# Kernel optimization log

Hardware: AMD Instinct MI355X
Metric: run time of the kernel (lower is better)

The kernel has to match this reference:

```python
import jax, jax.numpy as jnp
import numpy as np

SCALE = 0.0078125  # dequant scale from init_kwargs


def setup_inputs() -> dict:
    key = jax.random.key(0)
    k1, k2, k3 = jax.random.split(key, 3)
    B, S, D_IN, D_OUT = 4, 2048, 2048, 8192
    x = jax.random.normal(k1, (B, S, D_IN), dtype=jnp.float32)
    weight = jax.random.normal(k2, (D_OUT, D_IN), dtype=jnp.float32)  # torch Linear layout
    bias = jax.random.normal(k3, (D_OUT,), dtype=jnp.float32)
    return {"x": x, "weight": weight, "bias": bias}


def reference(x, weight, bias):
    # MATMUL.apply(x, weight.t(), bias, scale): scaled matmul + fused bias
    # out[b,s,o] = scale * sum_i x[b,s,i] * weight[o,i] + bias[o]
    out = jnp.einsum('bsi,oi->bso', x, weight) * jnp.asarray(SCALE, x.dtype)
    return out + bias
```

## Files before the change

kernel.cpp:

```cpp
#include <hip/hip_runtime.h>
#include <hip/hip_bf16.h>
#include <stdint.h>

typedef __bf16 bf16x8 __attribute__((ext_vector_type(8)));
typedef float  f32x4  __attribute__((ext_vector_type(4)));

static constexpr float kScale = 0.0078125f;

static __device__ __forceinline__ uint32_t bf16_rne(float f) {
  uint32_t u = __builtin_bit_cast(uint32_t, f);
  u += 0x7FFFu + ((u >> 16) & 1u);
  return u >> 16;
}
static __device__ __forceinline__ uint32_t pack2(float lo, float hi) {
  return bf16_rne(lo) | (bf16_rne(hi) << 16);
}

__global__ __launch_bounds__(256) void cvt_f32_to_bf16(
    const float* __restrict__ src, uint4* __restrict__ dst) {
  const int i = blockIdx.x * 256 + threadIdx.x;
  const float4* sv = reinterpret_cast<const float4*>(src);
  float4 a = sv[2 * i];
  float4 b = sv[2 * i + 1];
  uint4 o;
  o.x = pack2(a.x, a.y);
  o.y = pack2(a.z, a.w);
  o.z = pack2(b.x, b.y);
  o.w = pack2(b.z, b.w);
  dst[i] = o;
}

static __device__ __forceinline__ void gload_lds16(const void* g, void* l) {
  __builtin_amdgcn_global_load_lds(
      (const __attribute__((address_space(1))) void*)g,
      (__attribute__((address_space(3))) void*)l, 16, 0, 0);
}

#define BARRIER() __builtin_amdgcn_s_barrier()
#define LGKM0()                                        \
  do {                                                 \
    asm volatile("s_waitcnt lgkmcnt(0)" ::: "memory"); \
    __builtin_amdgcn_sched_barrier(0);                 \
  } while (0)
#define VM6()                                          \
  do {                                                 \
    asm volatile("s_waitcnt vmcnt(6)" ::: "memory");   \
    __builtin_amdgcn_sched_barrier(0);                 \
  } while (0)

template <int MH, int NH>
__device__ __forceinline__ void quad(f32x4 (&acc)[8][4],
                                     const bf16x8 (&aF)[4][2],
                                     const bf16x8 (&bF)[2][2]) {
#pragma unroll
  for (int mi = 0; mi < 4; ++mi)
#pragma unroll
    for (int ni = 0; ni < 2; ++ni)
#pragma unroll
      for (int kk = 0; kk < 2; ++kk)
        acc[MH * 4 + mi][NH * 2 + ni] = __builtin_amdgcn_mfma_f32_16x16x32_bf16(
            aF[mi][kk], bF[ni][kk], acc[MH * 4 + mi][NH * 2 + ni], 0, 0, 0);
}

__global__ __launch_bounds__(512, 2) void gemm256_8phase(
    const uint16_t* __restrict__ A, const uint16_t* __restrict__ B,
    const float* __restrict__ bias, float* __restrict__ C,
    int Mi, int Ni, int Ki) {
  __shared__ __align__(16) uint16_t As[2][256 * 64];
  __shared__ __align__(16) uint16_t Bs[2][256 * 64];

  const int tid = threadIdx.x;
  const int l   = tid & 63;
  const int wv  = tid >> 6;
  const int wr  = wv >> 2;
  const int wc  = wv & 3;
  const int fr  = l & 15;
  const int fh  = l >> 4;
  const int l8  = l >> 3;
  const int l7  = l & 7;

  const int nbm = Mi >> 8, nbn = Ni >> 8;
  const int nwg = nbm * nbn;
  const int q = nwg >> 3, r = nwg & 7;
  const int xcd = (int)blockIdx.x & 7, orig = (int)blockIdx.x >> 3;
  const int swz = (xcd < r ? xcd * (q + 1) : r * (q + 1) + (xcd - r) * q) + orig;
  const int bm = swz / nbn;
  const int bn = swz % nbn;

  const int xcol = (l7 ^ l8) << 3;
  const uint16_t* gA0 = A + (size_t)((bm << 8) + (wv << 3) + l8) * Ki + xcol;
  const int bw0 = ((wv & 3) << 3) + ((wv >> 2) << 6);
  const uint16_t* gB0 = B + (size_t)((bn << 8) + bw0 + l8) * Ki + xcol;

#define STAGE_A(bufi, chunk, t)                              \
  gload_lds16(gA0 + (size_t)(chunk) * Ki + (t) * 64,         \
              &As[bufi][(size_t)((chunk) + (wv << 3)) << 6])
#define STAGE_B(bufi, roff, t)                               \
  gload_lds16(gB0 + (size_t)(roff) * Ki + (t) * 64,          \
              &Bs[bufi][(size_t)(bw0 + (roff)) << 6])

  const int ac0 = fh ^ (fr & 7);
  const bf16x8* Av = reinterpret_cast<const bf16x8*>(&As[0][0]);
  const bf16x8* Bv = reinterpret_cast<const bf16x8*>(&Bs[0][0]);
  constexpr int TILE_V = (256 * 64) / 8;

#define LDA_(bufi, mh, mi, kk)                                              \
  Av[(bufi) * TILE_V + (((wr << 7) + ((mh) << 6) + ((mi) << 4) + fr) << 3) + \
     (ac0 ^ ((kk) << 2))]
#define LDB_(bufi, nh, ni, kk)                                              \
  Bv[(bufi) * TILE_V + (((wc << 6) + ((nh) << 5) + ((ni) << 4) + fr) << 3) + \
     (ac0 ^ ((kk) << 2))]

  f32x4 acc[8][4] = {};
  bf16x8 aF[4][2], b0[2][2], b1[2][2];

  const int NT = Ki >> 6;
  const int NI = NT >> 1;

  STAGE_A(0, 0, 0);
  STAGE_B(0, 0, 0);
  STAGE_A(0, 128, 0);
  STAGE_B(0, 128, 0);
  STAGE_B(0, 32, 0);
  STAGE_B(0, 160, 0);
  STAGE_A(0, 64, 0);
  STAGE_A(0, 192, 0);
  STAGE_A(1, 0, 1);
  STAGE_B(1, 0, 1);
  asm volatile("s_waitcnt vmcnt(6)" ::: "memory");
  __builtin_amdgcn_sched_barrier(0);
  BARRIER();

#pragma unroll 1
  for (int i = 0; i < NI; ++i) {
    const int t1 = 2 * i + 1, t2 = 2 * i + 2, t3 = 2 * i + 3;
    const bool g2 = (t2 < NT), g3 = (t3 < NT);

#pragma unroll
    for (int mi = 0; mi < 4; ++mi) {
      aF[mi][0] = LDA_(0, 0, mi, 0);
      aF[mi][1] = LDA_(0, 0, mi, 1);
    }
#pragma unroll
    for (int ni = 0; ni < 2; ++ni) {
      b0[ni][0] = LDB_(0, 0, ni, 0);
      b0[ni][1] = LDB_(0, 0, ni, 1);
    }
    STAGE_A(1, 128, t1);
    STAGE_B(1, 128, t1);
    VM6();
    BARRIER();
    LGKM0();
    __builtin_amdgcn_s_setprio(1);
    quad<0, 0>(acc, aF, b0);
    __builtin_amdgcn_s_setprio(0);
    BARRIER();

#pragma unroll
    for (int ni = 0; ni < 2; ++ni) {
      b1[ni][0] = LDB_(0, 1, ni, 0);
      b1[ni][1] = LDB_(0, 1, ni, 1);
    }
    STAGE_B(1, 32, t1);
    STAGE_B(1, 160, t1);
    VM6();
    BARRIER();
    LGKM0();
    __builtin_amdgcn_s_setprio(1);
    quad<0, 1>(acc, aF, b1);
    __builtin_amdgcn_s_setprio(0);
    BARRIER();

#pragma unroll
    for (int mi = 0; mi < 4; ++mi) {
      aF[mi][0] = LDA_(0, 1, mi, 0);
      aF[mi][1] = LDA_(0, 1, mi, 1);
    }
    STAGE_A(1, 64, t1);
    STAGE_A(1, 192, t1);
    VM6();
    BARRIER();
    LGKM0();
    __builtin_amdgcn_s_setprio(1);
    quad<1, 0>(acc, aF, b0);
    __builtin_amdgcn_s_setprio(0);
    BARRIER();

    if (g2) {
      STAGE_A(0, 0, t2);
      STAGE_B(0, 0, t2);
    }
    VM6();
    BARRIER();
    LGKM0();
    __builtin_amdgcn_s_setprio(1);
    quad<1, 1>(acc, aF, b1);
    __builtin_amdgcn_s_setprio(0);
    BARRIER();

#pragma unroll
    for (int mi = 0; mi < 4; ++mi) {
      aF[mi][0] = LDA_(1, 0, mi, 0);
      aF[mi][1] = LDA_(1, 0, mi, 1);
    }
#pragma unroll
    for (int ni = 0; ni < 2; ++ni) {
      b0[ni][0] = LDB_(1, 0, ni, 0);
      b0[ni][1] = LDB_(1, 0, ni, 1);
    }
    if (g2) {
      STAGE_A(0, 128, t2);
      STAGE_B(0, 128, t2);
    }
    VM6();
    BARRIER();
    LGKM0();
    __builtin_amdgcn_s_setprio(1);
    quad<0, 0>(acc, aF, b0);
    __builtin_amdgcn_s_setprio(0);
    BARRIER();

#pragma unroll
    for (int ni = 0; ni < 2; ++ni) {
      b1[ni][0] = LDB_(1, 1, ni, 0);
      b1[ni][1] = LDB_(1, 1, ni, 1);
    }
    if (g2) {
      STAGE_B(0, 32, t2);
      STAGE_B(0, 160, t2);
    }
    VM6();
    BARRIER();
    LGKM0();
    __builtin_amdgcn_s_setprio(1);
    quad<0, 1>(acc, aF, b1);
    __builtin_amdgcn_s_setprio(0);
    BARRIER();

#pragma unroll
    for (int mi = 0; mi < 4; ++mi) {
      aF[mi][0] = LDA_(1, 1, mi, 0);
      aF[mi][1] = LDA_(1, 1, mi, 1);
    }
    if (g2) {
      STAGE_A(0, 64, t2);
      STAGE_A(0, 192, t2);
    }
    VM6();
    BARRIER();
    LGKM0();
    __builtin_amdgcn_s_setprio(1);
    quad<1, 0>(acc, aF, b0);
    __builtin_amdgcn_s_setprio(0);
    BARRIER();

    if (g3) {
      STAGE_A(1, 0, t3);
      STAGE_B(1, 0, t3);
    }
    VM6();
    BARRIER();
    LGKM0();
    __builtin_amdgcn_s_setprio(1);
    quad<1, 1>(acc, aF, b1);
    __builtin_amdgcn_s_setprio(0);
    BARRIER();
  }

  const int rowB = (bm << 8) + (wr << 7);
  const int colB = (bn << 8) + (wc << 6);
#pragma unroll
  for (int n = 0; n < 4; ++n) {
    const int col = colB + n * 16 + fr;
    const float bv = bias[col];
#pragma unroll
    for (int m = 0; m < 8; ++m) {
      const int row = rowB + m * 16 + fh * 4;
#pragma unroll
      for (int j = 0; j < 4; ++j)
        C[(size_t)(row + j) * Ni + col] = acc[m][n][j] * kScale + bv;
    }
  }
}

__global__ __launch_bounds__(256) void gemm_bf16_bias(
    const uint16_t* __restrict__ A, const uint16_t* __restrict__ B,
    const float* __restrict__ bias, float* __restrict__ C,
    int Mi, int Ni, int Ki) {
  __shared__ __align__(16) uint16_t As[128 * 32];
  __shared__ __align__(16) uint16_t Bs[128 * 32];

  const int tid  = threadIdx.x;
  const int lane = tid & 63;
  const int wv   = tid >> 6;
  const int wr   = wv >> 1;
  const int wc   = wv & 1;
  const int fr   = lane & 15;
  const int fh   = lane >> 4;

  const int nTilesN = Ni >> 7;
  const int nwg = gridDim.x;
  const int q = nwg >> 3, r = nwg & 7;
  const int xcd = (int)blockIdx.x & 7, orig = (int)blockIdx.x >> 3;
  const int swz = (xcd < r ? xcd * (q + 1) : r * (q + 1) + (xcd - r) * q) + orig;
  const int bm = swz / nTilesN;
  const int bn = swz % nTilesN;

  const int sRow = tid >> 2;
  const int sCol = (tid & 3) << 3;

  const uint16_t* gA0 = A + (size_t)(bm * 128 + sRow) * Ki + sCol;
  const uint16_t* gA1 = gA0 + (size_t)64 * Ki;
  const uint16_t* gB0 = B + (size_t)(bn * 128 + sRow) * Ki + sCol;
  const uint16_t* gB1 = gB0 + (size_t)64 * Ki;
  uint16_t* lA0 = &As[tid * 8];
  uint16_t* lA1 = &As[(256 + tid) * 8];
  uint16_t* lB0 = &Bs[tid * 8];
  uint16_t* lB1 = &Bs[(256 + tid) * 8];

  const bf16x8* Av = reinterpret_cast<const bf16x8*>(As);
  const bf16x8* Bv = reinterpret_cast<const bf16x8*>(Bs);

  f32x4 acc[4][4] = {};

  for (int k0 = 0; k0 < Ki; k0 += 32) {
    gload_lds16(gA0 + k0, lA0);
    gload_lds16(gA1 + k0, lA1);
    gload_lds16(gB0 + k0, lB0);
    gload_lds16(gB1 + k0, lB1);
    __syncthreads();

    bf16x8 af[4], bfr[4];
#pragma unroll
    for (int m = 0; m < 4; ++m) af[m] = Av[(wr * 64 + m * 16 + fr) * 4 + fh];
#pragma unroll
    for (int n = 0; n < 4; ++n) bfr[n] = Bv[(wc * 64 + n * 16 + fr) * 4 + fh];

#pragma unroll
    for (int m = 0; m < 4; ++m)
#pragma unroll
      for (int n = 0; n < 4; ++n)
        acc[m][n] = __builtin_amdgcn_mfma_f32_16x16x32_bf16(af[m], bfr[n],
                                                            acc[m][n], 0, 0, 0);
    __syncthreads();
  }

  const int rowBase = bm * 128 + wr * 64;
  const int colBase = bn * 128 + wc * 64;
#pragma unroll
  for (int n = 0; n < 4; ++n) {
    const int col = colBase + n * 16 + fr;
    const float bv = bias[col];
#pragma unroll
    for (int m = 0; m < 4; ++m) {
      const int row = rowBase + m * 16 + fh * 4;
#pragma unroll
      for (int j = 0; j < 4; ++j)
        C[(size_t)(row + j) * Ni + col] = acc[m][n][j] * kScale + bv;
    }
  }
}

__global__ void naive_gemm(const float* __restrict__ x, const float* __restrict__ w,
                           const float* __restrict__ bias, float* __restrict__ out,
                           int Mi, int Ni, int Ki) {
  long idx = (long)blockIdx.x * blockDim.x + threadIdx.x;
  if (idx >= (long)Mi * Ni) return;
  int m = (int)(idx / Ni), n = (int)(idx % Ni);
  float s = 0.f;
  for (int k = 0; k < Ki; ++k) s += x[(long)m * Ki + k] * w[(long)n * Ki + k];
  out[idx] = s * kScale + bias[n];
}

extern "C" void kernel_launch(void* const* d_in, const int* in_sizes, int n_in,
                              void* d_out, int out_size, void* d_ws, size_t ws_size,
                              hipStream_t stream) {
  const float* x    = (const float*)d_in[0];
  const float* w    = (const float*)d_in[1];
  const float* bias = (const float*)d_in[2];
  float* out = (float*)d_out;

  const int Ni = in_sizes[2];
  const int Ki = in_sizes[1] / Ni;
  const int Mi = in_sizes[0] / Ki;

  const size_t nx = (size_t)Mi * Ki;
  const size_t nw = (size_t)Ni * Ki;

  if (ws_size >= (nx + nw) * sizeof(uint16_t) && (Ki % 32) == 0 &&
      (Mi % 128) == 0 && (Ni % 128) == 0) {
    uint16_t* xb = (uint16_t*)d_ws;
    uint16_t* wb = xb + nx;
    cvt_f32_to_bf16<<<(int)(nx / 2048), 256, 0, stream>>>(x, (uint4*)xb);
    cvt_f32_to_bf16<<<(int)(nw / 2048), 256, 0, stream>>>(w, (uint4*)wb);

    if ((Mi % 256) == 0 && (Ni % 256) == 0 && (Ki % 128) == 0) {
      dim3 grid((Mi / 256) * (Ni / 256));
      gemm256_8phase<<<grid, 512, 0, stream>>>(xb, wb, bias, out, Mi, Ni, Ki);
    } else {
      dim3 grid((Mi / 128) * (Ni / 128));
      gemm_bf16_bias<<<grid, 256, 0, stream>>>(xb, wb, bias, out, Mi, Ni, Ki);
    }
  } else {
    long total = (long)Mi * Ni;
    naive_gemm<<<(int)((total + 255) / 256), 256, 0, stream>>>(x, w, bias, out,
                                                               Mi, Ni, Ki);
  }
}
```

Baseline: 372.5 us.

## Restructure 8-phase GEMM pipeline with interleaved warp-to-tile mapping and peeled tail

Changes each wave's sub-tile mapping so a wave covers rows and columns split across the two halves of the 256x256 tile. The global-to-LDS staging is reordered to match, loading A and B in contiguous 64-row chunks at an earlier point in the schedule. Most phases drop the vmcnt wait and use a partial lgkmcnt wait, and the final iteration is peeled so the main loop needs no guards. The aim is to let more memory traffic overlap with MFMA work and to cut wait stalls. The cost is tighter correctness margins around buffer reuse ordering.

```diff
diff --git a/kernel.cpp b/kernel.cpp
--- a/kernel.cpp
+++ b/kernel.cpp
@@ -42,16 +42,20 @@
     asm volatile("s_waitcnt lgkmcnt(0)" ::: "memory"); \
     __builtin_amdgcn_sched_barrier(0);                 \
   } while (0)
-#define VM6()                                          \
-  do {                                                 \
-    asm volatile("s_waitcnt vmcnt(6)" ::: "memory");   \
-    __builtin_amdgcn_sched_barrier(0);                 \
+#define LGKM8() asm volatile("s_waitcnt lgkmcnt(8)" ::: "memory")
+#define VMW(n)                                               \
+  do {                                                       \
+    asm volatile("s_waitcnt vmcnt(" #n ")" ::: "memory");    \
+    __builtin_amdgcn_sched_barrier(0);                       \
   } while (0)
+
+constexpr int TILE_V = (256 * 64) / 8;
 
 template <int MH, int NH>
 __device__ __forceinline__ void quad(f32x4 (&acc)[8][4],
                                      const bf16x8 (&aF)[4][2],
                                      const bf16x8 (&bF)[2][2]) {
+  __builtin_amdgcn_s_setprio(1);
 #pragma unroll
   for (int mi = 0; mi < 4; ++mi)
 #pragma unroll
@@ -60,6 +64,28 @@
       for (int kk = 0; kk < 2; ++kk)
         acc[MH * 4 + mi][NH * 2 + ni] = __builtin_amdgcn_mfma_f32_16x16x32_bf16(
             aF[mi][kk], bF[ni][kk], acc[MH * 4 + mi][NH * 2 + ni], 0, 0, 0);
+  __builtin_amdgcn_s_setprio(0);
+}
+
+template <int BUF, int MH>
+__device__ __forceinline__ void loadA(bf16x8 (&aF)[4][2], const bf16x8* Av,
+                                      int wr, int fr, int ac0) {
+#pragma unroll
+  for (int mi = 0; mi < 4; ++mi) {
+    const int row = (MH << 7) + (wr << 6) + (mi << 4) + fr;
+    aF[mi][0] = Av[BUF * TILE_V + row * 8 + ac0];
+    aF[mi][1] = Av[BUF * TILE_V + row * 8 + (ac0 ^ 4)];
+  }
+}
+template <int BUF, int NH>
+__device__ __forceinline__ void loadB(bf16x8 (&bF)[2][2], const bf16x8* Bv,
+                                      int wc, int fr, int ac0) {
+#pragma unroll
+  for (int ni = 0; ni < 2; ++ni) {
+    const int row = (NH << 7) + (wc << 5) + (ni << 4) + fr;
+    bF[ni][0] = Bv[BUF * TILE_V + row * 8 + ac0];
+    bF[ni][1] = Bv[BUF * TILE_V + row * 8 + (ac0 ^ 4)];
+  }
 }
 
 __global__ __launch_bounds__(512, 2) void gemm256_8phase(
@@ -89,27 +115,18 @@
 
   const int xcol = (l7 ^ l8) << 3;
   const uint16_t* gA0 = A + (size_t)((bm << 8) + (wv << 3) + l8) * Ki + xcol;
-  const int bw0 = ((wv & 3) << 3) + ((wv >> 2) << 6);
-  const uint16_t* gB0 = B + (size_t)((bn << 8) + bw0 + l8) * Ki + xcol;
-
-#define STAGE_A(bufi, chunk, t)                              \
-  gload_lds16(gA0 + (size_t)(chunk) * Ki + (t) * 64,         \
-              &As[bufi][(size_t)((chunk) + (wv << 3)) << 6])
-#define STAGE_B(bufi, roff, t)                               \
-  gload_lds16(gB0 + (size_t)(roff) * Ki + (t) * 64,          \
-              &Bs[bufi][(size_t)(bw0 + (roff)) << 6])
+  const uint16_t* gB0 = B + (size_t)((bn << 8) + (wv << 3) + l8) * Ki + xcol;
+
+#define STAGE_A(bufi, chunk, t)                        \
+  gload_lds16(gA0 + (size_t)(chunk) * Ki + (t) * 64,   \
+              &As[bufi][((chunk) + (wv << 3)) << 6])
+#define STAGE_B(bufi, chunk, t)                        \
+  gload_lds16(gB0 + (size_t)(chunk) * Ki + (t) * 64,   \
+              &Bs[bufi][((chunk) + (wv << 3)) << 6])
 
   const int ac0 = fh ^ (fr & 7);
   const bf16x8* Av = reinterpret_cast<const bf16x8*>(&As[0][0]);
   const bf16x8* Bv = reinterpret_cast<const bf16x8*>(&Bs[0][0]);
-  constexpr int TILE_V = (256 * 64) / 8;
-
-#define LDA_(bufi, mh, mi, kk)                                              \
-  Av[(bufi) * TILE_V + (((wr << 7) + ((mh) << 6) + ((mi) << 4) + fr) << 3) + \
-     (ac0 ^ ((kk) << 2))]
-#define LDB_(bufi, nh, ni, kk)                                              \
-  Bv[(bufi) * TILE_V + (((wc << 6) + ((nh) << 5) + ((ni) << 4) + fr) << 3) + \
-     (ac0 ^ ((kk) << 2))]
 
   f32x4 acc[8][4] = {};
   bf16x8 aF[4][2], b0[2][2], b1[2][2];
@@ -117,165 +134,119 @@
   const int NT = Ki >> 6;
   const int NI = NT >> 1;
 
-  STAGE_A(0, 0, 0);
-  STAGE_B(0, 0, 0);
-  STAGE_A(0, 128, 0);
-  STAGE_B(0, 128, 0);
-  STAGE_B(0, 32, 0);
-  STAGE_B(0, 160, 0);
-  STAGE_A(0, 64, 0);
-  STAGE_A(0, 192, 0);
-  STAGE_A(1, 0, 1);
-  STAGE_B(1, 0, 1);
-  asm volatile("s_waitcnt vmcnt(6)" ::: "memory");
-  __builtin_amdgcn_sched_barrier(0);
+  STAGE_A(0, 0, 0);   STAGE_A(0, 64, 0);
+  STAGE_B(0, 0, 0);   STAGE_B(0, 64, 0);
+  STAGE_B(0, 128, 0); STAGE_B(0, 192, 0);
+  STAGE_A(0, 128, 0); STAGE_A(0, 192, 0);
+  STAGE_A(1, 0, 1);   STAGE_A(1, 64, 1);
+  STAGE_B(1, 0, 1);   STAGE_B(1, 64, 1);
+  STAGE_B(1, 128, 1); STAGE_B(1, 192, 1);
+  VMW(6);
   BARRIER();
 
 #pragma unroll 1
-  for (int i = 0; i < NI; ++i) {
+  for (int i = 0; i < NI - 1; ++i) {
     const int t1 = 2 * i + 1, t2 = 2 * i + 2, t3 = 2 * i + 3;
-    const bool g2 = (t2 < NT), g3 = (t3 < NT);
-
-#pragma unroll
-    for (int mi = 0; mi < 4; ++mi) {
-      aF[mi][0] = LDA_(0, 0, mi, 0);
-      aF[mi][1] = LDA_(0, 0, mi, 1);
-    }
-#pragma unroll
-    for (int ni = 0; ni < 2; ++ni) {
-      b0[ni][0] = LDB_(0, 0, ni, 0);
-      b0[ni][1] = LDB_(0, 0, ni, 1);
-    }
-    STAGE_A(1, 128, t1);
-    STAGE_B(1, 128, t1);
-    VM6();
-    BARRIER();
-    LGKM0();
-    __builtin_amdgcn_s_setprio(1);
+
+    loadA<0, 0>(aF, Av, wr, fr, ac0);
+    loadB<0, 0>(b0, Bv, wc, fr, ac0);
+    STAGE_A(1, 128, t1); STAGE_A(1, 192, t1);
+    LGKM8();
+    BARRIER(); LGKM0();
     quad<0, 0>(acc, aF, b0);
-    __builtin_amdgcn_s_setprio(0);
-    BARRIER();
-
-#pragma unroll
-    for (int ni = 0; ni < 2; ++ni) {
-      b1[ni][0] = LDB_(0, 1, ni, 0);
-      b1[ni][1] = LDB_(0, 1, ni, 1);
-    }
-    STAGE_B(1, 32, t1);
-    STAGE_B(1, 160, t1);
-    VM6();
-    BARRIER();
-    LGKM0();
-    __builtin_amdgcn_s_setprio(1);
+    BARRIER();
+
+    loadB<0, 1>(b1, Bv, wc, fr, ac0);
+    STAGE_A(0, 0, t2); STAGE_A(0, 64, t2);
+    BARRIER(); LGKM0();
     quad<0, 1>(acc, aF, b1);
-    __builtin_amdgcn_s_setprio(0);
-    BARRIER();
-
-#pragma unroll
-    for (int mi = 0; mi < 4; ++mi) {
-      aF[mi][0] = LDA_(0, 1, mi, 0);
-      aF[mi][1] = LDA_(0, 1, mi, 1);
-    }
-    STAGE_A(1, 64, t1);
-    STAGE_A(1, 192, t1);
-    VM6();
-    BARRIER();
-    LGKM0();
-    __builtin_amdgcn_s_setprio(1);
+    BARRIER();
+
+    loadA<0, 1>(aF, Av, wr, fr, ac0);
+    STAGE_B(0, 0, t2); STAGE_B(0, 64, t2);
+    BARRIER(); LGKM0();
     quad<1, 0>(acc, aF, b0);
-    __builtin_amdgcn_s_setprio(0);
-    BARRIER();
-
-    if (g2) {
-      STAGE_A(0, 0, t2);
-      STAGE_B(0, 0, t2);
-    }
-    VM6();
-    BARRIER();
-    LGKM0();
-    __builtin_amdgcn_s_setprio(1);
+    BARRIER();
+
+    STAGE_B(0, 128, t2); STAGE_B(0, 192, t2);
+    VMW(6);
+    BARRIER();
     quad<1, 1>(acc, aF, b1);
-    __builtin_amdgcn_s_setprio(0);
-    BARRIER();
-
-#pragma unroll
-    for (int mi = 0; mi < 4; ++mi) {
-      aF[mi][0] = LDA_(1, 0, mi, 0);
-      aF[mi][1] = LDA_(1, 0, mi, 1);
-    }
-#pragma unroll
-    for (int ni = 0; ni < 2; ++ni) {
-      b0[ni][0] = LDB_(1, 0, ni, 0);
-      b0[ni][1] = LDB_(1, 0, ni, 1);
-    }
-    if (g2) {
-      STAGE_A(0, 128, t2);
-      STAGE_B(0, 128, t2);
-    }
-    VM6();
-    BARRIER();
-    LGKM0();
-    __builtin_amdgcn_s_setprio(1);
+    BARRIER();
+
+    loadA<1, 0>(aF, Av, wr, fr, ac0);
+    loadB<1, 0>(b0, Bv, wc, fr, ac0);
+    STAGE_A(0, 128, t2); STAGE_A(0, 192, t2);
+    LGKM8();
+    BARRIER(); LGKM0();
     quad<0, 0>(acc, aF, b0);
-    __builtin_amdgcn_s_setprio(0);
-    BARRIER();
-
-#pragma unroll
-    for (int ni = 0; ni < 2; ++ni) {
-      b1[ni][0] = LDB_(1, 1, ni, 0);
-      b1[ni][1] = LDB_(1, 1, ni, 1);
-    }
-    if (g2) {
-      STAGE_B(0, 32, t2);
-      STAGE_B(0, 160, t2);
-    }
-    VM6();
-    BARRIER();
-    LGKM0();
-    __builtin_amdgcn_s_setprio(1);
+    BARRIER();
+
+    loadB<1, 1>(b1, Bv, wc, fr, ac0);
+    STAGE_A(1, 0, t3); STAGE_A(1, 64, t3);
+    BARRIER(); LGKM0();
     quad<0, 1>(acc, aF, b1);
-    __builtin_amdgcn_s_setprio(0);
-    BARRIER();
-
-#pragma unroll
-    for (int mi = 0; mi < 4; ++mi) {
-      aF[mi][0] = LDA_(1, 1, mi, 0);
-      aF[mi][1] = LDA_(1, 1, mi, 1);
-    }
-    if (g2) {
-      STAGE_A(0, 64, t2);
-      STAGE_A(0, 192, t2);
-    }
-    VM6();
-    BARRIER();
-    LGKM0();
-    __builtin_amdgcn_s_setprio(1);
+    BARRIER();
+
+    loadA<1, 1>(aF, Av, wr, fr, ac0);
+    STAGE_B(1, 0, t3); STAGE_B(1, 64, t3);
+    BARRIER(); LGKM0();
     quad<1, 0>(acc, aF, b0);
-    __builtin_amdgcn_s_setprio(0);
-    BARRIER();
-
-    if (g3) {
-      STAGE_A(1, 0, t3);
-      STAGE_B(1, 0, t3);
-    }
-    VM6();
-    BARRIER();
-    LGKM0();
-    __builtin_amdgcn_s_setprio(1);
+    BARRIER();
+
+    STAGE_B(1, 128, t3); STAGE_B(1, 192, t3);
+    VMW(6);
+    BARRIER();
     quad<1, 1>(acc, aF, b1);
-    __builtin_amdgcn_s_setprio(0);
-    BARRIER();
-  }
-
-  const int rowB = (bm << 8) + (wr << 7);
-  const int colB = (bn << 8) + (wc << 6);
+    BARRIER();
+  }
+
+  {
+    const int t1 = NT - 1;
+    loadA<0, 0>(aF, Av, wr, fr, ac0);
+    loadB<0, 0>(b0, Bv, wc, fr, ac0);
+    STAGE_A(1, 128, t1); STAGE_A(1, 192, t1);
+    LGKM8();
+    BARRIER(); LGKM0();
+    quad<0, 0>(acc, aF, b0);
+    BARRIER();
+    loadB<0, 1>(b1, Bv, wc, fr, ac0);
+    BARRIER(); LGKM0();
+    quad<0, 1>(acc, aF, b1);
+    BARRIER();
+    loadA<0, 1>(aF, Av, wr, fr, ac0);
+    BARRIER(); LGKM0();
+    quad<1, 0>(acc, aF, b0);
+    BARRIER();
+    VMW(0);
+    BARRIER();
+    quad<1, 1>(acc, aF, b1);
+    BARRIER();
+    loadA<1, 0>(aF, Av, wr, fr, ac0);
+    loadB<1, 0>(b0, Bv, wc, fr, ac0);
+    BARRIER(); LGKM0();
+    quad<0, 0>(acc, aF, b0);
+    BARRIER();
+    loadB<1, 1>(b1, Bv, wc, fr, ac0);
+    BARRIER(); LGKM0();
+    quad<0, 1>(acc, aF, b1);
+    BARRIER();
+    loadA<1, 1>(aF, Av, wr, fr, ac0);
+    BARRIER(); LGKM0();
+    quad<1, 0>(acc, aF, b0);
+    BARRIER();
+    quad<1, 1>(acc, aF, b1);
+  }
+
+  const int rowB = (bm << 8) + (wr << 6);
+  const int colB = (bn << 8) + (wc << 5);
 #pragma unroll
   for (int n = 0; n < 4; ++n) {
-    const int col = colB + n * 16 + fr;
+    const int col = colB + (n >> 1) * 128 + (n & 1) * 16 + fr;
     const float bv = bias[col];
 #pragma unroll
     for (int m = 0; m < 8; ++m) {
-      const int row = rowB + m * 16 + fh * 4;
+      const int row = rowB + (m >> 2) * 128 + (m & 3) * 16 + fh * 4;
 #pragma unroll
       for (int j = 0; j < 4; ++j)
         C[(size_t)(row + j) * Ni + col] = acc[m][n][j] * kScale + bv;
@@ -394,7 +365,7 @@
     cvt_f32_to_bf16<<<(int)(nx / 2048), 256, 0, stream>>>(x, (uint4*)xb);
     cvt_f32_to_bf16<<<(int)(nw / 2048), 256, 0, stream>>>(w, (uint4*)wb);
 
-    if ((Mi % 256) == 0 && (Ni % 256) == 0 && (Ki % 128) == 0) {
+    if ((Mi % 256) == 0 && (Ni % 256) == 0 && (Ki % 128) == 0 && Ki >= 256) {
       dim3 grid((Mi / 256) * (Ni / 256));
       gemm256_8phase<<<grid, 512, 0, stream>>>(xb, wb, bias, out, Mi, Ni, Ki);
     } else {
```

New measurement: 382.0 us. +2.6%, slower.
